# Performance work log

Measured on AMD Instinct MI355X. Metric: run time of the kernel, lower is better.

## Reference

```python
import jax, jax.numpy as jnp
import numpy as np

H, D = 4, 32            # heads, head_dim
HID = H * D             # hidden_channels = 128
L = 2                   # num_layers
N = (100000, 50000)     # (n_session, n_item)
E = 200000              # edges per relation
ETYPES = ((0, 1), (1, 0), (1, 1))  # (src_type, dst_type) per relation


def _seg_softmax(alpha, dst, num_dst):
    # alpha: [E, H]; softmax over edges sharing the same dst node
    amax = jax.ops.segment_max(alpha, dst, num_segments=num_dst)
    amax = jnp.where(jnp.isfinite(amax), amax, 0.0)
    ex = jnp.exp(alpha - amax[dst])
    s = jax.ops.segment_sum(ex, dst, num_segments=num_dst)
    return ex / (s[dst] + 1e-16)


def _hgt_conv(xs, Wk, bk, Wq, bq, Wv, bv, Wa, ba, skip, a_rel, m_rel, p_rel, edges):
    # per-node-type k/q/v projections, reshaped to [N_t, H, D]
    k = [(x @ Wk[t] + bk[t]).reshape(-1, H, D) for t, x in enumerate(xs)]
    q = [(x @ Wq[t] + bq[t]).reshape(-1, H, D) for t, x in enumerate(xs)]
    v = [(x @ Wv[t] + bv[t]).reshape(-1, H, D) for t, x in enumerate(xs)]
    agg = [jnp.zeros((N[t], H, D), xs[0].dtype) for t in range(len(xs))]
    scale = 1.0 / jnp.sqrt(jnp.asarray(D, xs[0].dtype))
    for r, ((st, dt), (src, dst)) in enumerate(zip(ETYPES, edges)):
        kr = jnp.einsum('nhd,hde->nhe', k[st], a_rel[r])  # relation-specific key
        vr = jnp.einsum('nhd,hde->nhe', v[st], m_rel[r])  # relation-specific value
        alpha = jnp.einsum('ehd,ehd->eh', q[dt][dst], kr[src]) * p_rel[r] * scale
        alpha = _seg_softmax(alpha, dst, N[dt])
        msg = vr[src] * alpha[..., None]                  # [E, H, D]
        agg[dt] = agg[dt] + jax.ops.segment_sum(msg, dst, num_segments=N[dt])
    out = []
    for t in range(len(xs)):
        o = jax.nn.gelu(agg[t].reshape(N[t], HID), approximate=False) @ Wa[t] + ba[t]
        a = jax.nn.sigmoid(skip[t])
        out.append(a * o + (1.0 - a) * xs[t])
    return out


def setup_inputs() -> dict:
    key = jax.random.key(0)
    ks = jax.random.split(key, 16)
    f_in = 128
    s = 1.0 / np.sqrt(HID)
    return {
        'x0': jax.random.normal(ks[0], (N[0], f_in), jnp.float32),
        'x1': jax.random.normal(ks[1], (N[1], f_in), jnp.float32),
        'src0': jax.random.randint(ks[2], (E,), 0, N[0], jnp.int32),
        'dst0': jax.random.randint(ks[3], (E,), 0, N[1], jnp.int32),
        'src1': jax.random.randint(ks[4], (E,), 0, N[1], jnp.int32),
        'dst1': jax.random.randint(ks[5], (E,), 0, N[0], jnp.int32),
        'src2': jax.random.randint(ks[6], (E,), 0, N[1], jnp.int32),
        'dst2': jax.random.randint(ks[7], (E,), 0, N[1], jnp.int32),
        'W_in': jax.random.normal(ks[8], (2, f_in, HID), jnp.float32) / np.sqrt(f_in),
        'b_in': jnp.zeros((2, HID), jnp.float32),
        'Wk': jax.random.normal(ks[9], (L, 2, HID, HID), jnp.float32) * s,
        'bk': jnp.zeros((L, 2, HID), jnp.float32),
        'Wq': jax.random.normal(ks[10], (L, 2, HID, HID), jnp.float32) * s,
        'bq': jnp.zeros((L, 2, HID), jnp.float32),
        'Wv': jax.random.normal(ks[11], (L, 2, HID, HID), jnp.float32) * s,
        'bv': jnp.zeros((L, 2, HID), jnp.float32),
        'Wa': jax.random.normal(ks[12], (L, 2, HID, HID), jnp.float32) * s,
        'ba': jnp.zeros((L, 2, HID), jnp.float32),
        'skip': jnp.ones((L, 2), jnp.float32),
        'a_rel': jax.random.normal(ks[13], (L, 3, H, D, D), jnp.float32) / np.sqrt(D),
        'm_rel': jax.random.normal(ks[14], (L, 3, H, D, D), jnp.float32) / np.sqrt(D),
        'p_rel': jnp.ones((L, 3, H), jnp.float32),
    }


def reference(x0, x1, src0, dst0, src1, dst1, src2, dst2,
              W_in, b_in, Wk, bk, Wq, bq, Wv, bv, Wa, ba, skip,
              a_rel, m_rel, p_rel):
    edges = ((src0, dst0), (src1, dst1), (src2, dst2))
    h = [jax.nn.relu(x0 @ W_in[0] + b_in[0]),
         jax.nn.relu(x1 @ W_in[1] + b_in[1])]
    outs = [h]
    for l in range(L):
        h = _hgt_conv(h, Wk[l], bk[l], Wq[l], bq[l], Wv[l], bv[l],
                      Wa[l], ba[l], skip[l], a_rel[l], m_rel[l], p_rel[l], edges)
        outs.append(h)
    y0 = jnp.concatenate([o[0] for o in outs], axis=1)  # [N0, HID*(L+1)]
    y1 = jnp.concatenate([o[1] for o in outs], axis=1)  # [N1, HID*(L+1)]
    return (y0, y1)
```

## Files before the change

kernel.cpp:

```cpp
#include <hip/hip_runtime.h>
#include <math.h>


#define HID 128
#define OLD 384

typedef __attribute__((ext_vector_type(8))) short short8;
typedef __attribute__((ext_vector_type(4))) float f32x4;

__device__ __forceinline__ unsigned short f2b(float f) {
    unsigned u = __float_as_uint(f);
    u += 0x7fffu + ((u >> 16) & 1u);
    return (unsigned short)(u >> 16);
}
__device__ __forceinline__ unsigned pk2(float a, float b) {
    return (unsigned)f2b(a) | ((unsigned)f2b(b) << 16);
}
__device__ __forceinline__ float blo(unsigned u) { return __uint_as_float(u << 16); }
__device__ __forceinline__ float bhi(unsigned u) { return __uint_as_float(u & 0xffff0000u); }
__device__ __forceinline__ float b2f(unsigned short s) {
    return __uint_as_float((unsigned)s << 16);
}
__device__ __forceinline__ float gelu_f(float x) {
    return 0.5f * x * (1.0f + erff(x * 0.70710678118654752f));
}

template <int AFP32, int EPI>
__global__ __launch_bounds__(256) void mfma_gemm(
    const void* __restrict__ Aptr, int lda,
    const unsigned short* __restrict__ Wp,
    const float* __restrict__ biasP,
    unsigned short* __restrict__ Cb, int ldcb,
    float* __restrict__ Cf, int ldcf,
    const unsigned short* __restrict__ Hb,
    const float* __restrict__ skipP,
    int M)
{
    const int tid  = threadIdx.x;
    const int wid  = tid >> 6;
    const int lane = tid & 63;
    const int ow = (wid >> 1) * 64;
    const int nw = (wid & 1) * 64;
    const int lm = lane & 15;
    const int kq = lane >> 4;
    const int r0 = blockIdx.y * 128;
    const int ct = blockIdx.x;

    short8 wf[4][4];
    const unsigned short* wbase = Wp + (size_t)ct * 16384;
#pragma unroll
    for (int mi = 0; mi < 4; ++mi) {
        const int mt = (ow >> 4) + mi;
#pragma unroll
        for (int kt = 0; kt < 4; ++kt)
            wf[mi][kt] = *(const short8*)(wbase + (((mt * 4 + kt) * 64 + lane) << 3));
    }

    f32x4 acc[4][4];
#pragma unroll
    for (int ni = 0; ni < 4; ++ni)
#pragma unroll
        for (int mi = 0; mi < 4; ++mi)
            acc[ni][mi] = (f32x4){0.f, 0.f, 0.f, 0.f};

#pragma unroll
    for (int ni = 0; ni < 4; ++ni) {
        int node = r0 + nw + ni * 16 + lm;
        node = (node < M) ? node : (M - 1);
        short8 bfr[4];
        if (AFP32) {
            const float* ar = (const float*)Aptr + (size_t)node * lda;
#pragma unroll
            for (int kt = 0; kt < 4; ++kt) {
                float4 v0 = *(const float4*)(ar + kt * 32 + kq * 8);
                float4 v1 = *(const float4*)(ar + kt * 32 + kq * 8 + 4);
                short8 t;
                t[0] = (short)f2b(v0.x); t[1] = (short)f2b(v0.y);
                t[2] = (short)f2b(v0.z); t[3] = (short)f2b(v0.w);
                t[4] = (short)f2b(v1.x); t[5] = (short)f2b(v1.y);
                t[6] = (short)f2b(v1.z); t[7] = (short)f2b(v1.w);
                bfr[kt] = t;
            }
        } else {
            const unsigned short* ar = (const unsigned short*)Aptr + (size_t)node * lda;
#pragma unroll
            for (int kt = 0; kt < 4; ++kt)
                bfr[kt] = *(const short8*)(ar + kt * 32 + kq * 8);
        }
#pragma unroll
        for (int kt = 0; kt < 4; ++kt)
#pragma unroll
            for (int mi = 0; mi < 4; ++mi)
                acc[ni][mi] = __builtin_amdgcn_mfma_f32_16x16x32_bf16(
                    wf[mi][kt], bfr[kt], acc[ni][mi], 0, 0, 0);
    }

    float4 b4[4];
#pragma unroll
    for (int mi = 0; mi < 4; ++mi)
        b4[mi] = *(const float4*)(biasP + ct * 128 + ow + mi * 16 + kq * 4);

    float aa = 0.f, ab = 0.f;
    if (EPI == 2) {
        const float sv = *skipP;
        aa = 1.0f / (1.0f + __expf(-sv));
        ab = 1.0f - aa;
    }

#pragma unroll
    for (int ni = 0; ni < 4; ++ni) {
        const int node = r0 + nw + ni * 16 + lm;
        if (node >= M) continue;
#pragma unroll
        for (int mi = 0; mi < 4; ++mi) {
            const int oc = ow + mi * 16 + kq * 4;
            float v0 = acc[ni][mi][0] + b4[mi].x;
            float v1 = acc[ni][mi][1] + b4[mi].y;
            float v2 = acc[ni][mi][2] + b4[mi].z;
            float v3 = acc[ni][mi][3] + b4[mi].w;
            if (EPI == 1) {
                v0 = fmaxf(v0, 0.f); v1 = fmaxf(v1, 0.f);
                v2 = fmaxf(v2, 0.f); v3 = fmaxf(v3, 0.f);
            }
            if (EPI == 2) {
                uint2 hp = *(const uint2*)(Hb + (size_t)node * 128 + oc);
                v0 = aa * v0 + ab * blo(hp.x);
                v1 = aa * v1 + ab * bhi(hp.x);
                v2 = aa * v2 + ab * blo(hp.y);
                v3 = aa * v3 + ab * bhi(hp.y);
            }
            if (EPI != 0) {
                *(float4*)(Cf + (size_t)node * ldcf + oc) =
                    make_float4(v0, v1, v2, v3);
                *(uint2*)(Cb + (size_t)node * 128 + oc) =
                    make_uint2(pk2(v0, v1), pk2(v2, v3));
            } else {
                *(uint2*)(Cb + (size_t)node * ldcb + ct * 128 + oc) =
                    make_uint2(pk2(v0, v1), pk2(v2, v3));
            }
        }
    }
}

__device__ __forceinline__ void attn_loop(
    const unsigned short* __restrict__ kv, size_t ldkv, int kof, int vof,
    const int* __restrict__ rowptr, const int* __restrict__ esrc,
    int n, int lane, float q0, float q1,
    float& o0, float& o1)
{
    const int p0 = rowptr[n], p1 = rowptr[n + 1];
    float m = -INFINITY, l = 0.f, a0 = 0.f, a1 = 0.f;
    for (int p = p0; p < p1; ++p) {
        const int s = esrc[p];
        const size_t sb = (size_t)s * ldkv;
        const unsigned kp = *(const unsigned*)(kv + sb + kof + 2 * lane);
        const unsigned vp = *(const unsigned*)(kv + sb + vof + 2 * lane);
        float al = q0 * blo(kp) + q1 * bhi(kp);
        al += __shfl_xor(al, 1, 64);
        al += __shfl_xor(al, 2, 64);
        al += __shfl_xor(al, 4, 64);
        al += __shfl_xor(al, 8, 64);
        const float nm  = fmaxf(m, al);
        const float scl = __expf(m - nm);
        const float w   = __expf(al - nm);
        l  = l * scl + w;
        a0 = a0 * scl + w * blo(vp);
        a1 = a1 * scl + w * bhi(vp);
        m  = nm;
    }
    const float inv = 1.0f / (l + 1e-16f);
    o0 = a0 * inv;
    o1 = a1 * inv;
}

__global__ __launch_bounds__(256) void hgt_attn_t0(
    const unsigned short* __restrict__ qkv0,
    const unsigned short* __restrict__ qkv1,
    const int* __restrict__ rowptr, const int* __restrict__ esrc,
    unsigned short* __restrict__ agg, int N)
{
    const int wid = threadIdx.x >> 6, lane = threadIdx.x & 63;
    const int n = blockIdx.x * 4 + wid;
    if (n >= N) return;
    const unsigned qp = *(const unsigned*)(qkv0 + (size_t)n * 384 + 2 * lane);
    float o0, o1;
    attn_loop(qkv1, 640, 128, 256, rowptr, esrc, n, lane, blo(qp), bhi(qp), o0, o1);
    *(unsigned*)(agg + (size_t)n * 128 + 2 * lane) = pk2(gelu_f(o0), gelu_f(o1));
}

__global__ __launch_bounds__(256) void hgt_attn_t1(
    const unsigned short* __restrict__ qkv0,
    const unsigned short* __restrict__ qkv1,
    const int* __restrict__ rowptr0, const int* __restrict__ esrc0,
    const int* __restrict__ rowptr2, const int* __restrict__ esrc2,
    unsigned short* __restrict__ agg, int N)
{
    const int wid = threadIdx.x >> 6, lane = threadIdx.x & 63;
    const int n = blockIdx.x * 4 + wid;
    if (n >= N) return;
    const unsigned qp = *(const unsigned*)(qkv1 + (size_t)n * 640 + 2 * lane);
    const float q0 = blo(qp), q1 = bhi(qp);
    float x0, x1, y0, y1;
    attn_loop(qkv0, 384, 128, 256, rowptr0, esrc0, n, lane, q0, q1, x0, x1);
    attn_loop(qkv1, 640, 384, 512, rowptr2, esrc2, n, lane, q0, q1, y0, y1);
    *(unsigned*)(agg + (size_t)n * 128 + 2 * lane) =
        pk2(gelu_f(x0 + y0), gelu_f(x1 + y1));
}

__global__ void hgt_pack(
    const float* __restrict__ W_in, const float* __restrict__ b_in,
    const float* __restrict__ Wk, const float* __restrict__ bk,
    const float* __restrict__ Wq, const float* __restrict__ bq,
    const float* __restrict__ Wv, const float* __restrict__ bv,
    const float* __restrict__ Wa, const float* __restrict__ ba,
    const float* __restrict__ a_rel, const float* __restrict__ m_rel,
    const float* __restrict__ p_rel,
    unsigned short* __restrict__ Bp, float* __restrict__ bp)
{
    const int bid = blockIdx.x;
    const float* Wsrc = nullptr;
    const float* bsrc = nullptr;
    int l = -1, r = 0, kv = 0;
    if      (bid <  2) { Wsrc = W_in + (size_t)bid * 16384; bsrc = b_in + bid * 128; }
    else if (bid == 2) { Wsrc = Wq;                bsrc = bq; }
    else if (bid <= 4) { l = 0; r = 0; kv = bid - 3; }
    else if (bid == 5) { Wsrc = Wq + 16384;        bsrc = bq + 128; }
    else if (bid <= 7) { l = 0; r = 1; kv = bid - 6; }
    else if (bid <= 9) { l = 0; r = 2; kv = bid - 8; }
    else if (bid == 10){ Wsrc = Wa;                bsrc = ba; }
    else if (bid == 11){ Wsrc = Wa + 16384;        bsrc = ba + 128; }
    else if (bid == 12){ Wsrc = Wq + 2 * 16384;    bsrc = bq + 256; }
    else if (bid <= 14){ l = 1; r = 0; kv = bid - 13; }
    else if (bid == 15){ Wsrc = Wq + 3 * 16384;    bsrc = bq + 384; }
    else if (bid <= 17){ l = 1; r = 1; kv = bid - 16; }
    else if (bid <= 19){ l = 1; r = 2; kv = bid - 18; }
    else if (bid == 20){ Wsrc = Wa + 2 * 16384;    bsrc = ba + 256; }
    else               { Wsrc = Wa + 3 * 16384;    bsrc = ba + 384; }

    const bool iscw = (l >= 0);
    const float* rel = nullptr;
    if (iscw) {
        const int st = (r == 0) ? 0 : 1;
        Wsrc = (kv ? Wv : Wk) + (size_t)(l * 2 + st) * 16384;
        bsrc = (kv ? bv : bk) + (l * 2 + st) * 128;
        rel  = (kv ? m_rel : a_rel) + (size_t)(l * 3 + r) * 4096;
    }

    for (int i = threadIdx.x; i < 16384; i += 256) {
        const int mt = i >> 11, kt = (i >> 9) & 3, ln = (i >> 3) & 63, j = i & 7;
        const int m = mt * 16 + (ln & 15);
        const int k = kt * 32 + (ln >> 4) * 8 + j;
        float v;
        if (!iscw) {
            v = Wsrc[k * 128 + m];
        } else {
            const int h = m >> 5, e = m & 31;
            const float fac = kv ? 1.0f
                : p_rel[(l * 3 + r) * 4 + h] * 0.17677669529663687f;
            const float* wr = Wsrc + (size_t)k * 128 + h * 32;
            const float* rc = rel + h * 1024 + e;
            float s = 0.f;
#pragma unroll
            for (int d = 0; d < 32; ++d) s = fmaf(wr[d], rc[d * 32], s);
            v = s * fac;
        }
        Bp[(size_t)bid * 16384 + i] = f2b(v);
    }
    if (threadIdx.x < 128) {
        const int n = threadIdx.x;
        float v;
        if (!iscw) {
            v = bsrc[n];
        } else {
            const int h = n >> 5, e = n & 31;
            const float fac = kv ? 1.0f
                : p_rel[(l * 3 + r) * 4 + h] * 0.17677669529663687f;
            const float* rc = rel + h * 1024 + e;
            float s = 0.f;
#pragma unroll
            for (int d = 0; d < 32; ++d) s = fmaf(bsrc[h * 32 + d], rc[d * 32], s);
            v = s * fac;
        }
        bp[bid * 128 + n] = v;
    }
}

__global__ void hgt_hist(const int* __restrict__ d0, const int* __restrict__ d1,
                         const int* __restrict__ d2, int E, int N0v, int N1v,
                         int* __restrict__ deg)
{
    const int r = blockIdx.y;
    const int e = blockIdx.x * 256 + threadIdx.x;
    if (e >= E) return;
    const int* dd = (r == 0) ? d0 : (r == 1) ? d1 : d2;
    const int doff = (r == 0) ? 0 : (r == 1) ? N1v : (N1v + N0v);
    atomicAdd(&deg[doff + dd[e]], 1);
}

__global__ void hgt_scan1(const int* __restrict__ deg, int* __restrict__ rowptr,
                          int* __restrict__ bsums, int N0v, int N1v)
{
    const int r = blockIdx.y;
    const int Nd = (r == 1) ? N0v : N1v;
    const int n  = Nd + 1;
    if (blockIdx.x * 512 >= n) return;
    const int doff = (r == 0) ? 0 : (r == 1) ? N1v : (N1v + N0v);
    const int roff = (r == 0) ? 0 : (r == 1) ? (N1v + 1) : (N1v + N0v + 2);
    __shared__ int s[512];
    const int tid = threadIdx.x;
    const int i = blockIdx.x * 512 + tid;
    const int v = (i < Nd) ? deg[doff + i] : 0;
    s[tid] = v;
    __syncthreads();
    for (int off = 1; off < 512; off <<= 1) {
        const int t = (tid >= off) ? s[tid - off] : 0;
        __syncthreads();
        s[tid] += t;
        __syncthreads();
    }
    if (i < n) rowptr[roff + i] = s[tid] - v;
    if (tid == 511) bsums[r * 256 + blockIdx.x] = s[511];
}

__global__ void hgt_scan2(int* __restrict__ bsums)
{
    const int r = blockIdx.x;
    __shared__ int s[256];
    const int t = threadIdx.x;
    const int v = bsums[r * 256 + t];
    s[t] = v;
    __syncthreads();
    for (int off = 1; off < 256; off <<= 1) {
        const int u = (t >= off) ? s[t - off] : 0;
        __syncthreads();
        s[t] += u;
        __syncthreads();
    }
    bsums[r * 256 + t] = s[t] - v;
}

__global__ void hgt_scan3(int* __restrict__ rowptr, const int* __restrict__ bsums,
                          int N0v, int N1v)
{
    const int r = blockIdx.y;
    const int n = ((r == 1) ? N0v : N1v) + 1;
    const int i = blockIdx.x * 512 + threadIdx.x;
    if (i >= n) return;
    const int roff = (r == 0) ? 0 : (r == 1) ? (N1v + 1) : (N1v + N0v + 2);
    rowptr[roff + i] += bsums[r * 256 + blockIdx.x];
}

__global__ void hgt_fill(const int* __restrict__ s0, const int* __restrict__ d0,
                         const int* __restrict__ s1, const int* __restrict__ d1,
                         const int* __restrict__ s2, const int* __restrict__ d2,
                         int E, int N0v, int N1v,
                         const int* __restrict__ rowptr, int* __restrict__ cnt,
                         int* __restrict__ esrc)
{
    const int r = blockIdx.y;
    const int e = blockIdx.x * 256 + threadIdx.x;
    if (e >= E) return;
    const int* ss = (r == 0) ? s0 : (r == 1) ? s1 : s2;
    const int* dd = (r == 0) ? d0 : (r == 1) ? d1 : d2;
    const int doff = (r == 0) ? 0 : (r == 1) ? N1v : (N1v + N0v);
    const int roff = (r == 0) ? 0 : (r == 1) ? (N1v + 1) : (N1v + N0v + 2);
    const int d = dd[e];
    const int pos = atomicAdd(&cnt[doff + d], 1);
    esrc[(size_t)r * E + rowptr[roff + d] + pos] = ss[e];
}

extern "C" void kernel_launch(void* const* d_in, const int* in_sizes, int n_in,
                              void* d_out, int out_size, void* d_ws, size_t ws_size,
                              hipStream_t stream)
{
    const float* x0  = (const float*)d_in[0];
    const float* x1  = (const float*)d_in[1];
    const int* src0 = (const int*)d_in[2];
    const int* dst0 = (const int*)d_in[3];
    const int* src1 = (const int*)d_in[4];
    const int* dst1 = (const int*)d_in[5];
    const int* src2 = (const int*)d_in[6];
    const int* dst2 = (const int*)d_in[7];
    const float* W_in = (const float*)d_in[8];
    const float* b_in = (const float*)d_in[9];
    const float* Wk = (const float*)d_in[10];
    const float* bk = (const float*)d_in[11];
    const float* Wq = (const float*)d_in[12];
    const float* bq = (const float*)d_in[13];
    const float* Wv = (const float*)d_in[14];
    const float* bv = (const float*)d_in[15];
    const float* Wa = (const float*)d_in[16];
    const float* ba = (const float*)d_in[17];
    const float* skip = (const float*)d_in[18];
    const float* a_rel = (const float*)d_in[19];
    const float* m_rel = (const float*)d_in[20];
    const float* p_rel = (const float*)d_in[21];

    const int N0 = in_sizes[0] / HID;
    const int N1 = in_sizes[1] / HID;
    const int E  = in_sizes[2];
    float* out = (float*)d_out;
    (void)n_in; (void)out_size; (void)ws_size;

    char* p = (char*)d_ws;
    auto carve = [&](size_t bytes) -> char* {
        char* q = p;
        p += (bytes + 255) & ~(size_t)255;
        return q;
    };
    unsigned short* hbf  = (unsigned short*)carve((size_t)(N0 + N1) * 128 * 2);
    unsigned short* qkv0 = (unsigned short*)carve((size_t)N0 * 384 * 2);
    unsigned short* qkv1 = (unsigned short*)carve((size_t)N1 * 640 * 2);
    unsigned short* agg  = (unsigned short*)carve((size_t)(N0 + N1) * 128 * 2);
    unsigned short* packW = (unsigned short*)carve((size_t)22 * 16384 * 2);
    float* packb = (float*)carve((size_t)22 * 128 * 4);
    int* rowptr = (int*)carve((size_t)(N0 + 2 * N1 + 3) * 4);
    int* esrc   = (int*)carve((size_t)3 * E * 4);
    char* zbase = carve(0);
    int* deg   = (int*)carve((size_t)(N0 + 2 * N1) * 4);
    int* cnt   = (int*)carve((size_t)(N0 + 2 * N1) * 4);
    int* bsums = (int*)carve(3 * 256 * 4);
    const size_t zbytes = (size_t)((char*)(bsums + 3 * 256) - zbase);

    unsigned short* hbf1 = hbf + (size_t)N0 * 128;
    unsigned short* agg0 = agg;
    unsigned short* agg1 = agg + (size_t)N0 * 128;
    const int* rp0 = rowptr;
    const int* rp1 = rowptr + (N1 + 1);
    const int* rp2 = rowptr + (N1 + N0 + 2);
    const int* es0 = esrc;
    const int* es1 = esrc + (size_t)E;
    const int* es2 = esrc + (size_t)2 * E;

    hipMemsetAsync(zbase, 0, zbytes, stream);
    const int eb = (E + 255) / 256;
    const int nbx = (N0 + 1 + 511) / 512;
    hgt_hist <<<dim3(eb, 3), 256, 0, stream>>>(dst0, dst1, dst2, E, N0, N1, deg);
    hgt_scan1<<<dim3(nbx, 3), 512, 0, stream>>>(deg, rowptr, bsums, N0, N1);
    hgt_scan2<<<3, 256, 0, stream>>>(bsums);
    hgt_scan3<<<dim3(nbx, 3), 512, 0, stream>>>(rowptr, bsums, N0, N1);
    hgt_fill <<<dim3(eb, 3), 256, 0, stream>>>(src0, dst0, src1, dst1, src2, dst2,
                                               E, N0, N1, rowptr, cnt, (int*)esrc);

    hgt_pack<<<22, 256, 0, stream>>>(W_in, b_in, Wk, bk, Wq, bq, Wv, bv, Wa, ba,
                                     a_rel, m_rel, p_rel, packW, packb);

    auto mb = [](int M) { return (M + 127) / 128; };

    mfma_gemm<1, 1><<<dim3(1, mb(N0)), 256, 0, stream>>>(
        x0, 128, packW + 0 * 16384, packb + 0 * 128,
        hbf, 128, out, OLD, nullptr, nullptr, N0);
    mfma_gemm<1, 1><<<dim3(1, mb(N1)), 256, 0, stream>>>(
        x1, 128, packW + 1 * 16384, packb + 1 * 128,
        hbf1, 128, out + (size_t)N0 * OLD, OLD, nullptr, nullptr, N1);

    for (int l = 0; l < 2; ++l) {
        const int qkv0_blk = l ? 12 : 2;
        const int qkv1_blk = l ? 15 : 5;
        const int out0_blk = l ? 20 : 10;
        const int out1_blk = l ? 21 : 11;

        mfma_gemm<0, 0><<<dim3(3, mb(N0)), 256, 0, stream>>>(
            hbf, 128, packW + (size_t)qkv0_blk * 16384, packb + qkv0_blk * 128,
            qkv0, 384, nullptr, 0, nullptr, nullptr, N0);
        mfma_gemm<0, 0><<<dim3(5, mb(N1)), 256, 0, stream>>>(
            hbf1, 128, packW + (size_t)qkv1_blk * 16384, packb + qkv1_blk * 128,
            qkv1, 640, nullptr, 0, nullptr, nullptr, N1);

        hgt_attn_t0<<<(N0 + 3) / 4, 256, 0, stream>>>(
            qkv0, qkv1, rp1, es1, agg0, N0);
        hgt_attn_t1<<<(N1 + 3) / 4, 256, 0, stream>>>(
            qkv0, qkv1, rp0, es0, rp2, es2, agg1, N1);

        mfma_gemm<0, 2><<<dim3(1, mb(N0)), 256, 0, stream>>>(
            agg0, 128, packW + (size_t)out0_blk * 16384, packb + out0_blk * 128,
            hbf, 128, out + (size_t)(l + 1) * 128, OLD,
            hbf, skip + l * 2 + 0, N0);
        mfma_gemm<0, 2><<<dim3(1, mb(N1)), 256, 0, stream>>>(
            agg1, 128, packW + (size_t)out1_blk * 16384, packb + out1_blk * 128,
            hbf1, 128, out + (size_t)N0 * OLD + (size_t)(l + 1) * 128, OLD,
            hbf1, skip + l * 2 + 1, N1);
    }
}
```

Baseline: 981.8 us.

## Merge per-type GEMM and attention launches, keep A fragments resident, prefetch edges

Each GEMM now covers both node types in one launch, selected by block index. The QKV GEMM loads its A fragments once into registers and loops over all output column tiles, instead of spreading tiles across grid x and reloading A for each. The two attention kernels are merged into one launch, and the edge loop prefetches the next source's k/v before working on the current one. The setup kernels are also merged: the histogram goes into the weight pack, scan2 and scan3 combine via a wave reduction, and fill runs alongside the input projection. This cuts launch count and redundant A reads, at the cost of higher register pressure, fewer blocks for the QKV GEMM, and branch divergence between the merged roles.

Result: faster. 872.1 us (-11.2%).

```diff
diff --git a/kernel.cpp b/kernel.cpp
--- a/kernel.cpp
+++ b/kernel.cpp
@@ -18,23 +18,47 @@
 }
 __device__ __forceinline__ float blo(unsigned u) { return __uint_as_float(u << 16); }
 __device__ __forceinline__ float bhi(unsigned u) { return __uint_as_float(u & 0xffff0000u); }
-__device__ __forceinline__ float b2f(unsigned short s) {
-    return __uint_as_float((unsigned)s << 16);
-}
 __device__ __forceinline__ float gelu_f(float x) {
     return 0.5f * x * (1.0f + erff(x * 0.70710678118654752f));
 }
 
-template <int AFP32, int EPI>
-__global__ __launch_bounds__(256) void mfma_gemm(
-    const void* __restrict__ Aptr, int lda,
-    const unsigned short* __restrict__ Wp,
-    const float* __restrict__ biasP,
-    unsigned short* __restrict__ Cb, int ldcb,
-    float* __restrict__ Cf, int ldcf,
-    const unsigned short* __restrict__ Hb,
+template <int AFP32>
+__device__ __forceinline__ void load_bfrag(short8 (&d)[4], const void* Aptr,
+                                           int lda, int node, int kq)
+{
+    if (AFP32) {
+        const float* ar = (const float*)Aptr + (size_t)node * lda;
+#pragma unroll
+        for (int kt = 0; kt < 4; ++kt) {
+            float4 v0 = *(const float4*)(ar + kt * 32 + kq * 8);
+            float4 v1 = *(const float4*)(ar + kt * 32 + kq * 8 + 4);
+            short8 t;
+            t[0] = (short)f2b(v0.x); t[1] = (short)f2b(v0.y);
+            t[2] = (short)f2b(v0.z); t[3] = (short)f2b(v0.w);
+            t[4] = (short)f2b(v1.x); t[5] = (short)f2b(v1.y);
+            t[6] = (short)f2b(v1.z); t[7] = (short)f2b(v1.w);
+            d[kt] = t;
+        }
+    } else {
+        const unsigned short* ar = (const unsigned short*)Aptr + (size_t)node * lda;
+#pragma unroll
+        for (int kt = 0; kt < 4; ++kt)
+            d[kt] = *(const short8*)(ar + kt * 32 + kq * 8);
+    }
+}
+
+template <int AFP32, int EPI, int BRES>
+__device__ __forceinline__ void gemm_body(
+    int yb,
+    const void* __restrict__ A0, const void* __restrict__ A1, int lda,
+    const unsigned short* __restrict__ Wp, const float* __restrict__ biasP,
+    int wblk0, int wblk1, int nct0, int nct1,
+    unsigned short* __restrict__ Cb0, unsigned short* __restrict__ Cb1,
+    int ldcb0, int ldcb1,
+    float* __restrict__ Cf0, float* __restrict__ Cf1, int ldcf,
+    const unsigned short* __restrict__ Hb0, const unsigned short* __restrict__ Hb1,
     const float* __restrict__ skipP,
-    int M)
+    int M0, int M1, int yb0)
 {
     const int tid  = threadIdx.x;
     const int wid  = tid >> 6;
@@ -43,103 +67,132 @@
     const int nw = (wid & 1) * 64;
     const int lm = lane & 15;
     const int kq = lane >> 4;
-    const int r0 = blockIdx.y * 128;
-    const int ct = blockIdx.x;
-
-    short8 wf[4][4];
-    const unsigned short* wbase = Wp + (size_t)ct * 16384;
-#pragma unroll
-    for (int mi = 0; mi < 4; ++mi) {
-        const int mt = (ow >> 4) + mi;
-#pragma unroll
-        for (int kt = 0; kt < 4; ++kt)
-            wf[mi][kt] = *(const short8*)(wbase + (((mt * 4 + kt) * 64 + lane) << 3));
-    }
-
-    f32x4 acc[4][4];
-#pragma unroll
-    for (int ni = 0; ni < 4; ++ni)
-#pragma unroll
-        for (int mi = 0; mi < 4; ++mi)
-            acc[ni][mi] = (f32x4){0.f, 0.f, 0.f, 0.f};
-
-#pragma unroll
-    for (int ni = 0; ni < 4; ++ni) {
-        int node = r0 + nw + ni * 16 + lm;
-        node = (node < M) ? node : (M - 1);
-        short8 bfr[4];
-        if (AFP32) {
-            const float* ar = (const float*)Aptr + (size_t)node * lda;
-#pragma unroll
-            for (int kt = 0; kt < 4; ++kt) {
-                float4 v0 = *(const float4*)(ar + kt * 32 + kq * 8);
-                float4 v1 = *(const float4*)(ar + kt * 32 + kq * 8 + 4);
-                short8 t;
-                t[0] = (short)f2b(v0.x); t[1] = (short)f2b(v0.y);
-                t[2] = (short)f2b(v0.z); t[3] = (short)f2b(v0.w);
-                t[4] = (short)f2b(v1.x); t[5] = (short)f2b(v1.y);
-                t[6] = (short)f2b(v1.z); t[7] = (short)f2b(v1.w);
-                bfr[kt] = t;
-            }
-        } else {
-            const unsigned short* ar = (const unsigned short*)Aptr + (size_t)node * lda;
-#pragma unroll
-            for (int kt = 0; kt < 4; ++kt)
-                bfr[kt] = *(const short8*)(ar + kt * 32 + kq * 8);
-        }
-#pragma unroll
-        for (int kt = 0; kt < 4; ++kt)
-#pragma unroll
-            for (int mi = 0; mi < 4; ++mi)
-                acc[ni][mi] = __builtin_amdgcn_mfma_f32_16x16x32_bf16(
-                    wf[mi][kt], bfr[kt], acc[ni][mi], 0, 0, 0);
-    }
-
-    float4 b4[4];
-#pragma unroll
-    for (int mi = 0; mi < 4; ++mi)
-        b4[mi] = *(const float4*)(biasP + ct * 128 + ow + mi * 16 + kq * 4);
+
+    const int t  = (yb >= yb0) ? 1 : 0;
+    const int r0 = (t ? (yb - yb0) : yb) * 128;
+    const int M    = t ? M1 : M0;
+    const int nct  = t ? nct1 : nct0;
+    const int wblk = t ? wblk1 : wblk0;
+    const void* Aptr = t ? A1 : A0;
+    unsigned short* Cb = t ? Cb1 : Cb0;
+    const int ldcb = t ? ldcb1 : ldcb0;
+    float* Cf = t ? Cf1 : Cf0;
+    const unsigned short* Hb = t ? Hb1 : Hb0;
+
+    short8 bres[4][4];
+    if (BRES) {
+#pragma unroll
+        for (int ni = 0; ni < 4; ++ni) {
+            int node = r0 + nw + ni * 16 + lm;
+            node = (node < M) ? node : (M - 1);
+            load_bfrag<AFP32>(bres[ni], Aptr, lda, node, kq);
+        }
+    }
 
     float aa = 0.f, ab = 0.f;
     if (EPI == 2) {
-        const float sv = *skipP;
+        const float sv = skipP[t];
         aa = 1.0f / (1.0f + __expf(-sv));
         ab = 1.0f - aa;
     }
 
-#pragma unroll
-    for (int ni = 0; ni < 4; ++ni) {
-        const int node = r0 + nw + ni * 16 + lm;
-        if (node >= M) continue;
+    for (int ct = 0; ct < nct; ++ct) {
+        const unsigned short* wbase = Wp + (size_t)(wblk + ct) * 16384;
+        short8 wf[4][4];
 #pragma unroll
         for (int mi = 0; mi < 4; ++mi) {
-            const int oc = ow + mi * 16 + kq * 4;
-            float v0 = acc[ni][mi][0] + b4[mi].x;
-            float v1 = acc[ni][mi][1] + b4[mi].y;
-            float v2 = acc[ni][mi][2] + b4[mi].z;
-            float v3 = acc[ni][mi][3] + b4[mi].w;
-            if (EPI == 1) {
-                v0 = fmaxf(v0, 0.f); v1 = fmaxf(v1, 0.f);
-                v2 = fmaxf(v2, 0.f); v3 = fmaxf(v3, 0.f);
+            const int mt = (ow >> 4) + mi;
+#pragma unroll
+            for (int kt = 0; kt < 4; ++kt)
+                wf[mi][kt] = *(const short8*)(wbase + (((mt * 4 + kt) * 64 + lane) << 3));
+        }
+
+        f32x4 acc[4][4];
+#pragma unroll
+        for (int ni = 0; ni < 4; ++ni)
+#pragma unroll
+            for (int mi = 0; mi < 4; ++mi)
+                acc[ni][mi] = (f32x4){0.f, 0.f, 0.f, 0.f};
+
+#pragma unroll
+        for (int ni = 0; ni < 4; ++ni) {
+            if (BRES) {
+#pragma unroll
+                for (int kt = 0; kt < 4; ++kt)
+#pragma unroll
+                    for (int mi = 0; mi < 4; ++mi)
+                        acc[ni][mi] = __builtin_amdgcn_mfma_f32_16x16x32_bf16(
+                            wf[mi][kt], bres[ni][kt], acc[ni][mi], 0, 0, 0);
+            } else {
+                int node = r0 + nw + ni * 16 + lm;
+                node = (node < M) ? node : (M - 1);
+                short8 bl[4];
+                load_bfrag<AFP32>(bl, Aptr, lda, node, kq);
+#pragma unroll
+                for (int kt = 0; kt < 4; ++kt)
+#pragma unroll
+                    for (int mi = 0; mi < 4; ++mi)
+                        acc[ni][mi] = __builtin_amdgcn_mfma_f32_16x16x32_bf16(
+                            wf[mi][kt], bl[kt], acc[ni][mi], 0, 0, 0);
             }
-            if (EPI == 2) {
-                uint2 hp = *(const uint2*)(Hb + (size_t)node * 128 + oc);
-                v0 = aa * v0 + ab * blo(hp.x);
-                v1 = aa * v1 + ab * bhi(hp.x);
-                v2 = aa * v2 + ab * blo(hp.y);
-                v3 = aa * v3 + ab * bhi(hp.y);
+        }
+
+        float4 b4[4];
+#pragma unroll
+        for (int mi = 0; mi < 4; ++mi)
+            b4[mi] = *(const float4*)(biasP + (wblk + ct) * 128 + ow + mi * 16 + kq * 4);
+
+#pragma unroll
+        for (int ni = 0; ni < 4; ++ni) {
+            const int node = r0 + nw + ni * 16 + lm;
+            if (node >= M) continue;
+#pragma unroll
+            for (int mi = 0; mi < 4; ++mi) {
+                const int oc = ow + mi * 16 + kq * 4;
+                float v0 = acc[ni][mi][0] + b4[mi].x;
+                float v1 = acc[ni][mi][1] + b4[mi].y;
+                float v2 = acc[ni][mi][2] + b4[mi].z;
+                float v3 = acc[ni][mi][3] + b4[mi].w;
+                if (EPI == 1) {
+                    v0 = fmaxf(v0, 0.f); v1 = fmaxf(v1, 0.f);
+                    v2 = fmaxf(v2, 0.f); v3 = fmaxf(v3, 0.f);
+                }
+                if (EPI == 2) {
+                    uint2 hp = *(const uint2*)(Hb + (size_t)node * 128 + oc);
+                    v0 = aa * v0 + ab * blo(hp.x);
+                    v1 = aa * v1 + ab * bhi(hp.x);
+                    v2 = aa * v2 + ab * blo(hp.y);
+                    v3 = aa * v3 + ab * bhi(hp.y);
+                }
+                if (EPI != 0) {
+                    *(float4*)(Cf + (size_t)node * ldcf + oc) =
+                        make_float4(v0, v1, v2, v3);
+                    *(uint2*)(Cb + (size_t)node * 128 + oc) =
+                        make_uint2(pk2(v0, v1), pk2(v2, v3));
+                } else {
+                    *(uint2*)(Cb + (size_t)node * ldcb + ct * 128 + oc) =
+                        make_uint2(pk2(v0, v1), pk2(v2, v3));
+                }
             }
-            if (EPI != 0) {
-                *(float4*)(Cf + (size_t)node * ldcf + oc) =
-                    make_float4(v0, v1, v2, v3);
-                *(uint2*)(Cb + (size_t)node * 128 + oc) =
-                    make_uint2(pk2(v0, v1), pk2(v2, v3));
-            } else {
-                *(uint2*)(Cb + (size_t)node * ldcb + ct * 128 + oc) =
-                    make_uint2(pk2(v0, v1), pk2(v2, v3));
-            }
-        }
-    }
+        }
+    }
+}
+
+template <int AFP32, int EPI, int BRES>
+__global__ __launch_bounds__(256) void mfma_gemm(
+    const void* __restrict__ A0, const void* __restrict__ A1, int lda,
+    const unsigned short* __restrict__ Wp, const float* __restrict__ biasP,
+    int wblk0, int wblk1, int nct0, int nct1,
+    unsigned short* __restrict__ Cb0, unsigned short* __restrict__ Cb1,
+    int ldcb0, int ldcb1,
+    float* __restrict__ Cf0, float* __restrict__ Cf1, int ldcf,
+    const unsigned short* __restrict__ Hb0, const unsigned short* __restrict__ Hb1,
+    const float* __restrict__ skipP,
+    int M0, int M1, int yb0)
+{
+    gemm_body<AFP32, EPI, BRES>(blockIdx.x, A0, A1, lda, Wp, biasP,
+        wblk0, wblk1, nct0, nct1, Cb0, Cb1, ldcb0, ldcb1,
+        Cf0, Cf1, ldcf, Hb0, Hb1, skipP, M0, M1, yb0);
 }
 
 __device__ __forceinline__ void attn_loop(
@@ -150,64 +203,70 @@
 {
     const int p0 = rowptr[n], p1 = rowptr[n + 1];
     float m = -INFINITY, l = 0.f, a0 = 0.f, a1 = 0.f;
-    for (int p = p0; p < p1; ++p) {
-        const int s = esrc[p];
-        const size_t sb = (size_t)s * ldkv;
-        const unsigned kp = *(const unsigned*)(kv + sb + kof + 2 * lane);
-        const unsigned vp = *(const unsigned*)(kv + sb + vof + 2 * lane);
-        float al = q0 * blo(kp) + q1 * bhi(kp);
-        al += __shfl_xor(al, 1, 64);
-        al += __shfl_xor(al, 2, 64);
-        al += __shfl_xor(al, 4, 64);
-        al += __shfl_xor(al, 8, 64);
-        const float nm  = fmaxf(m, al);
-        const float scl = __expf(m - nm);
-        const float w   = __expf(al - nm);
-        l  = l * scl + w;
-        a0 = a0 * scl + w * blo(vp);
-        a1 = a1 * scl + w * bhi(vp);
-        m  = nm;
+    if (p0 < p1) {
+        const int s0 = esrc[p0];
+        const unsigned short* sp = kv + (size_t)s0 * ldkv + 2 * lane;
+        unsigned kp = *(const unsigned*)(sp + kof);
+        unsigned vp = *(const unsigned*)(sp + vof);
+        for (int p = p0; p < p1; ++p) {
+            const unsigned kc = kp, vc = vp;
+            if (p + 1 < p1) {
+                const int sn = esrc[p + 1];
+                const unsigned short* spn = kv + (size_t)sn * ldkv + 2 * lane;
+                kp = *(const unsigned*)(spn + kof);
+                vp = *(const unsigned*)(spn + vof);
+            }
+            float al = q0 * blo(kc) + q1 * bhi(kc);
+            al += __shfl_xor(al, 1, 64);
+            al += __shfl_xor(al, 2, 64);
+            al += __shfl_xor(al, 4, 64);
+            al += __shfl_xor(al, 8, 64);
+            const float nm  = fmaxf(m, al);
+            const float scl = __expf(m - nm);
+            const float w   = __expf(al - nm);
+            l  = l * scl + w;
+            a0 = a0 * scl + w * blo(vc);
+            a1 = a1 * scl + w * bhi(vc);
+            m  = nm;
+        }
     }
     const float inv = 1.0f / (l + 1e-16f);
     o0 = a0 * inv;
     o1 = a1 * inv;
 }
 
-__global__ __launch_bounds__(256) void hgt_attn_t0(
+__global__ __launch_bounds__(256) void hgt_attn(
     const unsigned short* __restrict__ qkv0,
     const unsigned short* __restrict__ qkv1,
-    const int* __restrict__ rowptr, const int* __restrict__ esrc,
-    unsigned short* __restrict__ agg, int N)
+    const int* __restrict__ rp1, const int* __restrict__ es1,
+    const int* __restrict__ rp0, const int* __restrict__ es0,
+    const int* __restrict__ rp2, const int* __restrict__ es2,
+    unsigned short* __restrict__ agg0, unsigned short* __restrict__ agg1,
+    int N0, int N1, int nb1)
 {
     const int wid = threadIdx.x >> 6, lane = threadIdx.x & 63;
-    const int n = blockIdx.x * 4 + wid;
-    if (n >= N) return;
-    const unsigned qp = *(const unsigned*)(qkv0 + (size_t)n * 384 + 2 * lane);
-    float o0, o1;
-    attn_loop(qkv1, 640, 128, 256, rowptr, esrc, n, lane, blo(qp), bhi(qp), o0, o1);
-    *(unsigned*)(agg + (size_t)n * 128 + 2 * lane) = pk2(gelu_f(o0), gelu_f(o1));
-}
-
-__global__ __launch_bounds__(256) void hgt_attn_t1(
-    const unsigned short* __restrict__ qkv0,
-    const unsigned short* __restrict__ qkv1,
-    const int* __restrict__ rowptr0, const int* __restrict__ esrc0,
-    const int* __restrict__ rowptr2, const int* __restrict__ esrc2,
-    unsigned short* __restrict__ agg, int N)
-{
-    const int wid = threadIdx.x >> 6, lane = threadIdx.x & 63;
-    const int n = blockIdx.x * 4 + wid;
-    if (n >= N) return;
-    const unsigned qp = *(const unsigned*)(qkv1 + (size_t)n * 640 + 2 * lane);
-    const float q0 = blo(qp), q1 = bhi(qp);
-    float x0, x1, y0, y1;
-    attn_loop(qkv0, 384, 128, 256, rowptr0, esrc0, n, lane, q0, q1, x0, x1);
-    attn_loop(qkv1, 640, 384, 512, rowptr2, esrc2, n, lane, q0, q1, y0, y1);
-    *(unsigned*)(agg + (size_t)n * 128 + 2 * lane) =
-        pk2(gelu_f(x0 + y0), gelu_f(x1 + y1));
-}
-
-__global__ void hgt_pack(
+    const int b = blockIdx.x;
+    if (b < nb1) {
+        const int n = b * 4 + wid;
+        if (n >= N1) return;
+        const unsigned qp = *(const unsigned*)(qkv1 + (size_t)n * 640 + 2 * lane);
+        const float q0 = blo(qp), q1 = bhi(qp);
+        float x0, x1, y0, y1;
+        attn_loop(qkv0, 384, 128, 256, rp0, es0, n, lane, q0, q1, x0, x1);
+        attn_loop(qkv1, 640, 384, 512, rp2, es2, n, lane, q0, q1, y0, y1);
+        *(unsigned*)(agg1 + (size_t)n * 128 + 2 * lane) =
+            pk2(gelu_f(x0 + y0), gelu_f(x1 + y1));
+    } else {
+        const int n = (b - nb1) * 4 + wid;
+        if (n >= N0) return;
+        const unsigned qp = *(const unsigned*)(qkv0 + (size_t)n * 384 + 2 * lane);
+        float o0, o1;
+        attn_loop(qkv1, 640, 128, 256, rp1, es1, n, lane, blo(qp), bhi(qp), o0, o1);
+        *(unsigned*)(agg0 + (size_t)n * 128 + 2 * lane) = pk2(gelu_f(o0), gelu_f(o1));
+    }
+}
+
+__global__ void hgt_prep(
     const float* __restrict__ W_in, const float* __restrict__ b_in,
     const float* __restrict__ Wk, const float* __restrict__ bk,
     const float* __restrict__ Wq, const float* __restrict__ bq,
@@ -215,9 +274,23 @@
     const float* __restrict__ Wa, const float* __restrict__ ba,
     const float* __restrict__ a_rel, const float* __restrict__ m_rel,
     const float* __restrict__ p_rel,
-    unsigned short* __restrict__ Bp, float* __restrict__ bp)
-{
+    unsigned short* __restrict__ Bp, float* __restrict__ bp,
+    const int* __restrict__ d0, const int* __restrict__ d1,
+    const int* __restrict__ d2, int E, int N0v, int N1v,
+    int* __restrict__ deg)
+{
+    if (blockIdx.y < 3) {
+        const int r = blockIdx.y;
+        const int e = blockIdx.x * 256 + threadIdx.x;
+        if (e >= E) return;
+        const int* dd = (r == 0) ? d0 : (r == 1) ? d1 : d2;
+        const int doff = (r == 0) ? 0 : (r == 1) ? N1v : (N1v + N0v);
+        atomicAdd(&deg[doff + dd[e]], 1);
+        return;
+    }
     const int bid = blockIdx.x;
+    if (bid >= 22) return;
+
     const float* Wsrc = nullptr;
     const float* bsrc = nullptr;
     int l = -1, r = 0, kv = 0;
@@ -285,18 +358,6 @@
     }
 }
 
-__global__ void hgt_hist(const int* __restrict__ d0, const int* __restrict__ d1,
-                         const int* __restrict__ d2, int E, int N0v, int N1v,
-                         int* __restrict__ deg)
-{
-    const int r = blockIdx.y;
-    const int e = blockIdx.x * 256 + threadIdx.x;
-    if (e >= E) return;
-    const int* dd = (r == 0) ? d0 : (r == 1) ? d1 : d2;
-    const int doff = (r == 0) ? 0 : (r == 1) ? N1v : (N1v + N0v);
-    atomicAdd(&deg[doff + dd[e]], 1);
-}
-
 __global__ void hgt_scan1(const int* __restrict__ deg, int* __restrict__ rowptr,
                           int* __restrict__ bsums, int N0v, int N1v)
 {
@@ -322,43 +383,50 @@
     if (tid == 511) bsums[r * 256 + blockIdx.x] = s[511];
 }
 
-__global__ void hgt_scan2(int* __restrict__ bsums)
-{
-    const int r = blockIdx.x;
-    __shared__ int s[256];
-    const int t = threadIdx.x;
-    const int v = bsums[r * 256 + t];
-    s[t] = v;
-    __syncthreads();
-    for (int off = 1; off < 256; off <<= 1) {
-        const int u = (t >= off) ? s[t - off] : 0;
-        __syncthreads();
-        s[t] += u;
-        __syncthreads();
-    }
-    bsums[r * 256 + t] = s[t] - v;
-}
-
-__global__ void hgt_scan3(int* __restrict__ rowptr, const int* __restrict__ bsums,
-                          int N0v, int N1v)
+__global__ void hgt_scan23(int* __restrict__ rowptr, const int* __restrict__ bsums,
+                           int N0v, int N1v)
 {
     const int r = blockIdx.y;
     const int n = ((r == 1) ? N0v : N1v) + 1;
-    const int i = blockIdx.x * 512 + threadIdx.x;
-    if (i >= n) return;
+    if (blockIdx.x * 512 >= n) return;
     const int roff = (r == 0) ? 0 : (r == 1) ? (N1v + 1) : (N1v + N0v + 2);
-    rowptr[roff + i] += bsums[r * 256 + blockIdx.x];
-}
-
-__global__ void hgt_fill(const int* __restrict__ s0, const int* __restrict__ d0,
-                         const int* __restrict__ s1, const int* __restrict__ d1,
-                         const int* __restrict__ s2, const int* __restrict__ d2,
-                         int E, int N0v, int N1v,
-                         const int* __restrict__ rowptr, int* __restrict__ cnt,
-                         int* __restrict__ esrc)
-{
-    const int r = blockIdx.y;
-    const int e = blockIdx.x * 256 + threadIdx.x;
+    const int tid = threadIdx.x;
+    int v = (tid < (int)blockIdx.x) ? bsums[r * 256 + tid] : 0;
+#pragma unroll
+    for (int o = 1; o < 64; o <<= 1) v += __shfl_xor(v, o, 64);
+    __shared__ int ws[8];
+    if ((tid & 63) == 0) ws[tid >> 6] = v;
+    __syncthreads();
+    int base = 0;
+#pragma unroll
+    for (int k = 0; k < 8; ++k) base += ws[k];
+    const int i = blockIdx.x * 512 + tid;
+    if (i < n) rowptr[roff + i] += base;
+}
+
+__global__ __launch_bounds__(256) void hgt_fill_inproj(
+    const int* __restrict__ s0, const int* __restrict__ d0,
+    const int* __restrict__ s1, const int* __restrict__ d1,
+    const int* __restrict__ s2, const int* __restrict__ d2,
+    int E, int N0v, int N1v,
+    const int* __restrict__ rowptr, int* __restrict__ cnt,
+    int* __restrict__ esrc, int eb,
+    const float* __restrict__ x0, const float* __restrict__ x1,
+    const unsigned short* __restrict__ Wp, const float* __restrict__ biasP,
+    unsigned short* __restrict__ hb0, unsigned short* __restrict__ hb1,
+    float* __restrict__ outp, int nGemm, int yb0)
+{
+    const int b = blockIdx.x;
+    if (b < nGemm) {
+        gemm_body<1, 1, 0>(b, x0, x1, 128, Wp, biasP, 0, 1, 1, 1,
+                           hb0, hb1, 128, 128,
+                           outp, outp + (size_t)N0v * OLD, OLD,
+                           nullptr, nullptr, nullptr, N0v, N1v, yb0);
+        return;
+    }
+    const int bb = b - nGemm;
+    const int r = bb / eb;
+    const int e = (bb - r * eb) * 256 + (int)threadIdx.x;
     if (e >= E) return;
     const int* ss = (r == 0) ? s0 : (r == 1) ? s1 : s2;
     const int* dd = (r == 0) ? d0 : (r == 1) ? d1 : d2;
@@ -432,27 +500,26 @@
     const int* es1 = esrc + (size_t)E;
     const int* es2 = esrc + (size_t)2 * E;
 
+    const int eb  = (E + 255) / 256;
+    const int nbx = (N0 + 1 + 511) / 512;
+    const int mbN0 = (N0 + 127) / 128;
+    const int mbN1 = (N1 + 127) / 128;
+    const int nGemm = mbN0 + mbN1;
+
     hipMemsetAsync(zbase, 0, zbytes, stream);
-    const int eb = (E + 255) / 256;
-    const int nbx = (N0 + 1 + 511) / 512;
-    hgt_hist <<<dim3(eb, 3), 256, 0, stream>>>(dst0, dst1, dst2, E, N0, N1, deg);
-    hgt_scan1<<<dim3(nbx, 3), 512, 0, stream>>>(deg, rowptr, bsums, N0, N1);
-    hgt_scan2<<<3, 256, 0, stream>>>(bsums);
-    hgt_scan3<<<dim3(nbx, 3), 512, 0, stream>>>(rowptr, bsums, N0, N1);
-    hgt_fill <<<dim3(eb, 3), 256, 0, stream>>>(src0, dst0, src1, dst1, src2, dst2,
-                                               E, N0, N1, rowptr, cnt, (int*)esrc);
-
-    hgt_pack<<<22, 256, 0, stream>>>(W_in, b_in, Wk, bk, Wq, bq, Wv, bv, Wa, ba,
-                                     a_rel, m_rel, p_rel, packW, packb);
-
-    auto mb = [](int M) { return (M + 127) / 128; };
-
-    mfma_gemm<1, 1><<<dim3(1, mb(N0)), 256, 0, stream>>>(
-        x0, 128, packW + 0 * 16384, packb + 0 * 128,
-        hbf, 128, out, OLD, nullptr, nullptr, N0);
-    mfma_gemm<1, 1><<<dim3(1, mb(N1)), 256, 0, stream>>>(
-        x1, 128, packW + 1 * 16384, packb + 1 * 128,
-        hbf1, 128, out + (size_t)N0 * OLD, OLD, nullptr, nullptr, N1);
+
+    hgt_prep<<<dim3(eb, 4), 256, 0, stream>>>(
+        W_in, b_in, Wk, bk, Wq, bq, Wv, bv, Wa, ba,
+        a_rel, m_rel, p_rel, packW, packb,
+        dst0, dst1, dst2, E, N0, N1, deg);
+
+    hgt_scan1 <<<dim3(nbx, 3), 512, 0, stream>>>(deg, rowptr, bsums, N0, N1);
+    hgt_scan23<<<dim3(nbx, 3), 512, 0, stream>>>(rowptr, bsums, N0, N1);
+
+    hgt_fill_inproj<<<nGemm + 3 * eb, 256, 0, stream>>>(
+        src0, dst0, src1, dst1, src2, dst2, E, N0, N1,
+        rowptr, cnt, (int*)esrc, eb,
+        x0, x1, packW, packb, hbf, hbf1, out, nGemm, mbN0);
 
     for (int l = 0; l < 2; ++l) {
         const int qkv0_blk = l ? 12 : 2;
@@ -460,25 +527,26 @@
         const int out0_blk = l ? 20 : 10;
         const int out1_blk = l ? 21 : 11;
 
-        mfma_gemm<0, 0><<<dim3(3, mb(N0)), 256, 0, stream>>>(
-            hbf, 128, packW + (size_t)qkv0_blk * 16384, packb + qkv0_blk * 128,
-            qkv0, 384, nullptr, 0, nullptr, nullptr, N0);
-        mfma_gemm<0, 0><<<dim3(5, mb(N1)), 256, 0, stream>>>(
-            hbf1, 128, packW + (size_t)qkv1_blk * 16384, packb + qkv1_blk * 128,
-            qkv1, 640, nullptr, 0, nullptr, nullptr, N1);
-
-        hgt_attn_t0<<<(N0 + 3) / 4, 256, 0, stream>>>(
-            qkv0, qkv1, rp1, es1, agg0, N0);
-        hgt_attn_t1<<<(N1 + 3) / 4, 256, 0, stream>>>(
-            qkv0, qkv1, rp0, es0, rp2, es2, agg1, N1);
-
-        mfma_gemm<0, 2><<<dim3(1, mb(N0)), 256, 0, stream>>>(
-            agg0, 128, packW + (size_t)out0_blk * 16384, packb + out0_blk * 128,
-            hbf, 128, out + (size_t)(l + 1) * 128, OLD,
-            hbf, skip + l * 2 + 0, N0);
-        mfma_gemm<0, 2><<<dim3(1, mb(N1)), 256, 0, stream>>>(
-            agg1, 128, packW + (size_t)out1_blk * 16384, packb + out1_blk * 128,
-            hbf1, 128, out + (size_t)N0 * OLD + (size_t)(l + 1) * 128, OLD,
-            hbf1, skip + l * 2 + 1, N1);
-    }
-}
+        mfma_gemm<0, 0, 1><<<nGemm, 256, 0, stream>>>(
+            hbf1, hbf, 128, packW, packb,
+            qkv1_blk, qkv0_blk, 5, 3,
+            qkv1, qkv0, 640, 384,
+            nullptr, nullptr, 0,
+            nullptr, nullptr, nullptr,
+            N1, N0, mbN1);
+
+        const int nb1 = (N1 + 3) / 4;
+        const int nb0 = (N0 + 3) / 4;
+        hgt_attn<<<nb1 + nb0, 256, 0, stream>>>(
+            qkv0, qkv1, rp1, es1, rp0, es0, rp2, es2,
+            agg0, agg1, N0, N1, nb1);
+
+        mfma_gemm<0, 2, 0><<<nGemm, 256, 0, stream>>>(
+            agg0, agg1, 128, packW, packb,
+            out0_blk, out1_blk, 1, 1,
+            hbf, hbf1, 128, 128,
+            out + (size_t)(l + 1) * 128,
+            out + (size_t)N0 * OLD + (size_t)(l + 1) * 128, OLD,
+            hbf, hbf1, skip + l * 2, N0, N1, mbN0);
+    }
+}
```
